# Performance work log

Hardware: AMD Instinct MI355X
Metric: run time of the kernel (lower is better)

Reference implementation:

```python
import jax, jax.numpy as jnp
import numpy as np

# --- HashGrid config (matches tcnn Encoding config in __init__) ---
N_LEVELS = 10
F = 8                       # n_features_per_level
LOG2_HASH = 20
HASH_SIZE = 1 << LOG2_HASH
BASE_RES = 16
MAX_RES = 1024
PER_LEVEL_SCALE = float(np.exp((np.log(MAX_RES) - np.log(BASE_RES)) / (N_LEVELS - 1)))
FEAT_DIM = 768
HIDDEN = FEAT_DIM // 2
N_POINTS = 131072

_PRIMES = (1, 2654435761)   # tcnn 2D spatial hash primes
_CORNERS = np.array([[0, 0], [1, 0], [0, 1], [1, 1]], dtype=np.uint32)


def _level_res(l):
    # tcnn: scale = base * growth^l - 1 ; resolution = ceil(scale) + 1
    scale = BASE_RES * PER_LEVEL_SCALE ** l - 1.0
    res = int(np.ceil(scale)) + 1
    return scale, res


def hashgrid_encode(coords, table):
    """coords: [N,2] in [0,1]; table: [L, HASH_SIZE, F] -> [N, L*F]."""
    corners = jnp.asarray(_CORNERS)                      # [4,2] uint32
    feats = []
    for l in range(N_LEVELS):
        scale, res = _level_res(l)
        pos = coords * jnp.float32(scale) + 0.5          # [N,2]
        pos_grid = jnp.floor(pos)
        frac = pos - pos_grid                            # [N,2]
        pg = pos_grid.astype(jnp.uint32)                 # [N,2]
        cpos = pg[:, None, :] + corners[None]            # [N,4,2]
        if res * res <= HASH_SIZE:
            # dense level: row-major index fits in the table
            idx = cpos[..., 0] + cpos[..., 1] * jnp.uint32(res)
        else:
            # spatial hash: (x*p0) ^ (y*p1) & (T-1)
            idx = (cpos[..., 0] * jnp.uint32(_PRIMES[0])) ^ (cpos[..., 1] * jnp.uint32(_PRIMES[1]))
            idx = idx & jnp.uint32(HASH_SIZE - 1)
        # bilinear weights: prod over dims of (frac if corner==1 else 1-frac)
        cf = corners[None].astype(frac.dtype)            # [1,4,2]
        w2 = jnp.where(cf == 1.0, frac[:, None, :], 1.0 - frac[:, None, :])  # [N,4,2]
        w = w2[..., 0] * w2[..., 1]                      # [N,4]
        lv = table[l][idx.astype(jnp.int32)]             # [N,4,F] irregular gather
        feats.append(jnp.einsum('nc,ncf->nf', w, lv))    # [N,F]
    return jnp.concatenate(feats, axis=-1)               # [N, L*F]


def setup_inputs() -> dict:
    key = jax.random.key(0)
    k0, k1, k2, k3 = jax.random.split(key, 4)
    coords = jax.random.uniform(k0, (N_POINTS, 2), dtype=jnp.float32)
    # tcnn initializes hash tables uniform in [-1e-4, 1e-4]
    table = jax.random.uniform(k1, (N_LEVELS, HASH_SIZE, F), dtype=jnp.float32,
                               minval=-1e-4, maxval=1e-4)
    in_dim = N_LEVELS * F
    w1 = jax.random.normal(k2, (in_dim, HIDDEN), dtype=jnp.float32) / np.sqrt(in_dim)
    b1 = jnp.zeros((HIDDEN,), dtype=jnp.float32)
    w2 = jax.random.normal(k3, (HIDDEN, FEAT_DIM), dtype=jnp.float32) / np.sqrt(HIDDEN)
    b2 = jnp.zeros((FEAT_DIM,), dtype=jnp.float32)
    return {"coords": coords, "table": table, "w1": w1, "b1": b1, "w2": w2, "b2": b2}


def reference(coords, table, w1, b1, w2, b2):
    enc = hashgrid_encode(coords, table)                 # [N, 80]
    h = jax.nn.relu(enc @ w1 + b1)                       # [N, 384]
    return h @ w2 + b2                                   # [N, 768]
```

## Files before the change

kernel.cpp:

```cpp
#include <hip/hip_runtime.h>
#include <cmath>

typedef short short8 __attribute__((ext_vector_type(8)));
typedef unsigned short u16x8 __attribute__((ext_vector_type(8)));
typedef float f32x4 __attribute__((ext_vector_type(4)));

struct EncParams { float scale[10]; int res[10]; };

__device__ __forceinline__ unsigned short f2bf(float f) {
  unsigned u = __builtin_bit_cast(unsigned, f);
  return (unsigned short)((u + 0x7FFFu + ((u >> 16) & 1u)) >> 16);
}

__device__ __forceinline__ void enc_level(float x, float y, float sc, int res,
    const float* __restrict__ table, int l, unsigned short* er) {
  float posx = __fadd_rn(__fmul_rn(x, sc), 0.5f);
  float posy = __fadd_rn(__fmul_rn(y, sc), 0.5f);
  float gx = floorf(posx), gy = floorf(posy);
  float fx = posx - gx, fy = posy - gy;
  unsigned px = (unsigned)gx, py = (unsigned)gy;
  unsigned idx[4];
  if (res * res <= (1 << 20)) {
    unsigned b = px + py * (unsigned)res;
    idx[0] = b; idx[1] = b + 1u;
    idx[2] = b + (unsigned)res; idx[3] = b + (unsigned)res + 1u;
  } else {
    unsigned hy0 = py * 2654435761u;
    unsigned hy1 = hy0 + 2654435761u;
    idx[0] = (px ^ hy0) & 0xFFFFFu;
    idx[1] = ((px + 1u) ^ hy0) & 0xFFFFFu;
    idx[2] = (px ^ hy1) & 0xFFFFFu;
    idx[3] = ((px + 1u) ^ hy1) & 0xFFFFFu;
  }
  float omx = 1.0f - fx, omy = 1.0f - fy;
  float w[4] = { omx * omy, fx * omy, omx * fy, fx * fy };
  const float4* tl = reinterpret_cast<const float4*>(table) + ((size_t)l << 21);
  float acc[8] = {0.f,0.f,0.f,0.f,0.f,0.f,0.f,0.f};
#pragma unroll
  for (int c = 0; c < 4; ++c) {
    float4 lo = tl[2 * (size_t)idx[c]];
    float4 hi = tl[2 * (size_t)idx[c] + 1];
    float wc = w[c];
    acc[0] = fmaf(wc, lo.x, acc[0]); acc[1] = fmaf(wc, lo.y, acc[1]);
    acc[2] = fmaf(wc, lo.z, acc[2]); acc[3] = fmaf(wc, lo.w, acc[3]);
    acc[4] = fmaf(wc, hi.x, acc[4]); acc[5] = fmaf(wc, hi.y, acc[5]);
    acc[6] = fmaf(wc, hi.z, acc[6]); acc[7] = fmaf(wc, hi.w, acc[7]);
  }
  u16x8 o;
#pragma unroll
  for (int j = 0; j < 8; ++j) o[j] = f2bf(acc[j]);
  *reinterpret_cast<u16x8*>(er + 8 * l) = o;
}

__global__ __launch_bounds__(512, 2) void nf_main(
    const float* __restrict__ coords, const float* __restrict__ table,
    const float* __restrict__ w1, const float* __restrict__ w2,
    const float* __restrict__ b1v, const float* __restrict__ b2v,
    float* __restrict__ out, EncParams P) {
  __shared__ __align__(16) unsigned short encS[128][104];
  __shared__ __align__(16) unsigned short hS[128][392];
  const int tid = threadIdx.x;
  const size_t rowBase = (size_t)blockIdx.x * 128;

  {
    const int p = tid & 127, g = tid >> 7;
    float2 c = reinterpret_cast<const float2*>(coords)[rowBase + p];
    unsigned short* er = &encS[p][0];
    if (g == 0) {
      enc_level(c.x, c.y, P.scale[0], P.res[0], table, 0, er);
      enc_level(c.x, c.y, P.scale[4], P.res[4], table, 4, er);
      enc_level(c.x, c.y, P.scale[8], P.res[8], table, 8, er);
    } else if (g == 1) {
      enc_level(c.x, c.y, P.scale[1], P.res[1], table, 1, er);
      enc_level(c.x, c.y, P.scale[5], P.res[5], table, 5, er);
      enc_level(c.x, c.y, P.scale[9], P.res[9], table, 9, er);
    } else if (g == 2) {
      enc_level(c.x, c.y, P.scale[2], P.res[2], table, 2, er);
      enc_level(c.x, c.y, P.scale[6], P.res[6], table, 6, er);
      u16x8 z = {};
      *reinterpret_cast<u16x8*>(er + 80) = z;
    } else {
      enc_level(c.x, c.y, P.scale[3], P.res[3], table, 3, er);
      enc_level(c.x, c.y, P.scale[7], P.res[7], table, 7, er);
      u16x8 z = {};
      *reinterpret_cast<u16x8*>(er + 88) = z;
    }
  }
  __syncthreads();

  const int lane = tid & 63, wv = tid >> 6;
  const int lr = lane & 15, lhi = lane >> 4;

  f32x4 acc1[8][3];
#pragma unroll
  for (int ri = 0; ri < 8; ++ri)
#pragma unroll
    for (int cf = 0; cf < 3; ++cf) acc1[ri][cf] = (f32x4){0.f, 0.f, 0.f, 0.f};
#pragma unroll
  for (int ks = 0; ks < 3; ++ks) {
    short8 a[8];
#pragma unroll
    for (int ri = 0; ri < 8; ++ri)
      a[ri] = *reinterpret_cast<const short8*>(&encS[16 * ri + lr][32 * ks + 8 * lhi]);
#pragma unroll
    for (int cf = 0; cf < 3; ++cf) {
      const int colB = 48 * wv + 16 * cf + lr;
      short8 b;
#pragma unroll
      for (int j = 0; j < 8; ++j) {
        int k = 32 * ks + 8 * lhi + j;
        b[j] = (k < 80) ? (short)f2bf(w1[(size_t)k * 384 + colB]) : (short)0;
      }
#pragma unroll
      for (int ri = 0; ri < 8; ++ri)
        acc1[ri][cf] = __builtin_amdgcn_mfma_f32_16x16x32_bf16(a[ri], b, acc1[ri][cf], 0, 0, 0);
    }
  }
#pragma unroll
  for (int ri = 0; ri < 8; ++ri)
#pragma unroll
    for (int cf = 0; cf < 3; ++cf) {
      int col = 48 * wv + 16 * cf + lr;
      float bb = b1v[col];
#pragma unroll
      for (int j = 0; j < 4; ++j) {
        int r = 16 * ri + 4 * lhi + j;
        float v = acc1[ri][cf][j] + bb;
        hS[r][col] = f2bf(fmaxf(v, 0.0f));
      }
    }
  __syncthreads();

#pragma unroll
  for (int cc = 0; cc < 2; ++cc) {
    f32x4 acc[8][3];
#pragma unroll
    for (int ri = 0; ri < 8; ++ri)
#pragma unroll
      for (int cf = 0; cf < 3; ++cf) acc[ri][cf] = (f32x4){0.f, 0.f, 0.f, 0.f};
#pragma unroll
    for (int ks = 0; ks < 12; ++ks) {
      short8 a[8];
#pragma unroll
      for (int ri = 0; ri < 8; ++ri)
        a[ri] = *reinterpret_cast<const short8*>(&hS[16 * ri + lr][32 * ks + 8 * lhi]);
#pragma unroll
      for (int cf = 0; cf < 3; ++cf) {
        const int colB = 96 * wv + 48 * cc + 16 * cf + lr;
        short8 b;
#pragma unroll
        for (int j = 0; j < 8; ++j) {
          int k = 32 * ks + 8 * lhi + j;
          b[j] = (short)f2bf(w2[(size_t)k * 768 + colB]);
        }
#pragma unroll
        for (int ri = 0; ri < 8; ++ri)
          acc[ri][cf] = __builtin_amdgcn_mfma_f32_16x16x32_bf16(a[ri], b, acc[ri][cf], 0, 0, 0);
      }
    }
#pragma unroll
    for (int ri = 0; ri < 8; ++ri)
#pragma unroll
      for (int cf = 0; cf < 3; ++cf) {
        int col = 96 * wv + 48 * cc + 16 * cf + lr;
        float bb = b2v[col];
#pragma unroll
        for (int j = 0; j < 4; ++j) {
          int r = 16 * ri + 4 * lhi + j;
          out[(rowBase + r) * 768 + col] = acc[ri][cf][j] + bb;
        }
      }
  }
}

extern "C" void kernel_launch(void* const* d_in, const int* in_sizes, int n_in,
                              void* d_out, int out_size, void* d_ws, size_t ws_size,
                              hipStream_t stream) {
  const float* coords = (const float*)d_in[0];
  const float* table  = (const float*)d_in[1];
  const float* w1     = (const float*)d_in[2];
  const float* b1     = (const float*)d_in[3];
  const float* w2     = (const float*)d_in[4];
  const float* b2     = (const float*)d_in[5];
  float* out = (float*)d_out;

  EncParams P;
  double pls = exp((log(1024.0) - log(16.0)) / 9.0);
  static const int RES[10] = {16, 26, 41, 65, 102, 162, 257, 407, 646, 1025};
  for (int l = 0; l < 10; ++l) {
    double sc = 16.0 * pow(pls, (double)l) - 1.0;
    P.scale[l] = (float)sc;
    P.res[l] = RES[l];
  }

  nf_main<<<1024, 512, 0, stream>>>(coords, table, w1, w2, b1, b2, out, P);
}
```

Measured before the change: 291.0 us.

## Batch hash-grid gathers and software-prefetch MLP weights ahead of MFMA

The encoder now computes indices for all of a thread's levels first and issues every table gather before any accumulation, so more loads are in flight at once. The W1 fragments are loaded before the barrier, overlapping with the encoding phase. In the second GEMM, the W2 fragments for the next k-step are prefetched into registers while the current step's MFMAs run. This targets global-load latency stalls but raises register pressure, which could cause spills under the 512-thread, 2-block launch bound.

```diff
diff --git a/kernel.cpp b/kernel.cpp
--- a/kernel.cpp
+++ b/kernel.cpp
@@ -12,44 +12,62 @@
   return (unsigned short)((u + 0x7FFFu + ((u >> 16) & 1u)) >> 16);
 }
 
-__device__ __forceinline__ void enc_level(float x, float y, float sc, int res,
-    const float* __restrict__ table, int l, unsigned short* er) {
-  float posx = __fadd_rn(__fmul_rn(x, sc), 0.5f);
-  float posy = __fadd_rn(__fmul_rn(y, sc), 0.5f);
-  float gx = floorf(posx), gy = floorf(posy);
-  float fx = posx - gx, fy = posy - gy;
-  unsigned px = (unsigned)gx, py = (unsigned)gy;
-  unsigned idx[4];
-  if (res * res <= (1 << 20)) {
-    unsigned b = px + py * (unsigned)res;
-    idx[0] = b; idx[1] = b + 1u;
-    idx[2] = b + (unsigned)res; idx[3] = b + (unsigned)res + 1u;
-  } else {
-    unsigned hy0 = py * 2654435761u;
-    unsigned hy1 = hy0 + 2654435761u;
-    idx[0] = (px ^ hy0) & 0xFFFFFu;
-    idx[1] = ((px + 1u) ^ hy0) & 0xFFFFFu;
-    idx[2] = (px ^ hy1) & 0xFFFFFu;
-    idx[3] = ((px + 1u) ^ hy1) & 0xFFFFFu;
-  }
-  float omx = 1.0f - fx, omy = 1.0f - fy;
-  float w[4] = { omx * omy, fx * omy, omx * fy, fx * fy };
-  const float4* tl = reinterpret_cast<const float4*>(table) + ((size_t)l << 21);
-  float acc[8] = {0.f,0.f,0.f,0.f,0.f,0.f,0.f,0.f};
-#pragma unroll
-  for (int c = 0; c < 4; ++c) {
-    float4 lo = tl[2 * (size_t)idx[c]];
-    float4 hi = tl[2 * (size_t)idx[c] + 1];
-    float wc = w[c];
-    acc[0] = fmaf(wc, lo.x, acc[0]); acc[1] = fmaf(wc, lo.y, acc[1]);
-    acc[2] = fmaf(wc, lo.z, acc[2]); acc[3] = fmaf(wc, lo.w, acc[3]);
-    acc[4] = fmaf(wc, hi.x, acc[4]); acc[5] = fmaf(wc, hi.y, acc[5]);
-    acc[6] = fmaf(wc, hi.z, acc[6]); acc[7] = fmaf(wc, hi.w, acc[7]);
-  }
-  u16x8 o;
-#pragma unroll
-  for (int j = 0; j < 8; ++j) o[j] = f2bf(acc[j]);
-  *reinterpret_cast<u16x8*>(er + 8 * l) = o;
+template<int NL>
+__device__ __forceinline__ void enc_levels(const float* __restrict__ table,
+    float x, float y, const float* sc, const int* rs, const int* lid,
+    unsigned short* er) {
+  unsigned idx[NL][4];
+  float w[NL][4];
+#pragma unroll
+  for (int t = 0; t < NL; ++t) {
+    float posx = __fadd_rn(__fmul_rn(x, sc[t]), 0.5f);
+    float posy = __fadd_rn(__fmul_rn(y, sc[t]), 0.5f);
+    float gx = floorf(posx), gy = floorf(posy);
+    float fx = posx - gx, fy = posy - gy;
+    unsigned px = (unsigned)gx, py = (unsigned)gy;
+    int res = rs[t];
+    if (res * res <= (1 << 20)) {
+      unsigned b = px + py * (unsigned)res;
+      idx[t][0] = b; idx[t][1] = b + 1u;
+      idx[t][2] = b + (unsigned)res; idx[t][3] = b + (unsigned)res + 1u;
+    } else {
+      unsigned hy0 = py * 2654435761u;
+      unsigned hy1 = hy0 + 2654435761u;
+      idx[t][0] = (px ^ hy0) & 0xFFFFFu;
+      idx[t][1] = ((px + 1u) ^ hy0) & 0xFFFFFu;
+      idx[t][2] = (px ^ hy1) & 0xFFFFFu;
+      idx[t][3] = ((px + 1u) ^ hy1) & 0xFFFFFu;
+    }
+    float omx = 1.0f - fx, omy = 1.0f - fy;
+    w[t][0] = omx * omy; w[t][1] = fx * omy;
+    w[t][2] = omx * fy;  w[t][3] = fx * fy;
+  }
+  float4 v[NL][4][2];
+#pragma unroll
+  for (int t = 0; t < NL; ++t) {
+    const float4* tl = reinterpret_cast<const float4*>(table) + ((size_t)lid[t] << 21);
+#pragma unroll
+    for (int c = 0; c < 4; ++c) {
+      v[t][c][0] = tl[2 * (size_t)idx[t][c]];
+      v[t][c][1] = tl[2 * (size_t)idx[t][c] + 1];
+    }
+  }
+#pragma unroll
+  for (int t = 0; t < NL; ++t) {
+    float acc[8] = {0.f,0.f,0.f,0.f,0.f,0.f,0.f,0.f};
+#pragma unroll
+    for (int c = 0; c < 4; ++c) {
+      float wc = w[t][c];
+      acc[0] = fmaf(wc, v[t][c][0].x, acc[0]); acc[1] = fmaf(wc, v[t][c][0].y, acc[1]);
+      acc[2] = fmaf(wc, v[t][c][0].z, acc[2]); acc[3] = fmaf(wc, v[t][c][0].w, acc[3]);
+      acc[4] = fmaf(wc, v[t][c][1].x, acc[4]); acc[5] = fmaf(wc, v[t][c][1].y, acc[5]);
+      acc[6] = fmaf(wc, v[t][c][1].z, acc[6]); acc[7] = fmaf(wc, v[t][c][1].w, acc[7]);
+    }
+    u16x8 o;
+#pragma unroll
+    for (int j = 0; j < 8; ++j) o[j] = f2bf(acc[j]);
+    *reinterpret_cast<u16x8*>(er + 8 * lid[t]) = o;
+  }
 }
 
 __global__ __launch_bounds__(512, 2) void nf_main(
@@ -61,35 +79,53 @@
   __shared__ __align__(16) unsigned short hS[128][392];
   const int tid = threadIdx.x;
   const size_t rowBase = (size_t)blockIdx.x * 128;
+  const int lane = tid & 63, wv = tid >> 6;
+  const int lr = lane & 15, lhi = lane >> 4;
 
   {
     const int p = tid & 127, g = tid >> 7;
     float2 c = reinterpret_cast<const float2*>(coords)[rowBase + p];
     unsigned short* er = &encS[p][0];
     if (g == 0) {
-      enc_level(c.x, c.y, P.scale[0], P.res[0], table, 0, er);
-      enc_level(c.x, c.y, P.scale[4], P.res[4], table, 4, er);
-      enc_level(c.x, c.y, P.scale[8], P.res[8], table, 8, er);
+      const int L[3] = {0, 4, 8};
+      const float sc[3] = {P.scale[0], P.scale[4], P.scale[8]};
+      const int rs[3] = {P.res[0], P.res[4], P.res[8]};
+      enc_levels<3>(table, c.x, c.y, sc, rs, L, er);
     } else if (g == 1) {
-      enc_level(c.x, c.y, P.scale[1], P.res[1], table, 1, er);
-      enc_level(c.x, c.y, P.scale[5], P.res[5], table, 5, er);
-      enc_level(c.x, c.y, P.scale[9], P.res[9], table, 9, er);
+      const int L[3] = {1, 5, 9};
+      const float sc[3] = {P.scale[1], P.scale[5], P.scale[9]};
+      const int rs[3] = {P.res[1], P.res[5], P.res[9]};
+      enc_levels<3>(table, c.x, c.y, sc, rs, L, er);
     } else if (g == 2) {
-      enc_level(c.x, c.y, P.scale[2], P.res[2], table, 2, er);
-      enc_level(c.x, c.y, P.scale[6], P.res[6], table, 6, er);
+      const int L[2] = {2, 6};
+      const float sc[2] = {P.scale[2], P.scale[6]};
+      const int rs[2] = {P.res[2], P.res[6]};
+      enc_levels<2>(table, c.x, c.y, sc, rs, L, er);
       u16x8 z = {};
       *reinterpret_cast<u16x8*>(er + 80) = z;
     } else {
-      enc_level(c.x, c.y, P.scale[3], P.res[3], table, 3, er);
-      enc_level(c.x, c.y, P.scale[7], P.res[7], table, 7, er);
+      const int L[2] = {3, 7};
+      const float sc[2] = {P.scale[3], P.scale[7]};
+      const int rs[2] = {P.res[3], P.res[7]};
+      enc_levels<2>(table, c.x, c.y, sc, rs, L, er);
       u16x8 z = {};
       *reinterpret_cast<u16x8*>(er + 88) = z;
     }
   }
+
+  short8 bW1[3][3];
+#pragma unroll
+  for (int ks = 0; ks < 3; ++ks)
+#pragma unroll
+    for (int cf = 0; cf < 3; ++cf) {
+      const int colB = 48 * wv + 16 * cf + lr;
+#pragma unroll
+      for (int j = 0; j < 8; ++j) {
+        int k = 32 * ks + 8 * lhi + j;
+        bW1[ks][cf][j] = (k < 80) ? (short)f2bf(w1[(size_t)k * 384 + colB]) : (short)0;
+      }
+    }
   __syncthreads();
-
-  const int lane = tid & 63, wv = tid >> 6;
-  const int lr = lane & 15, lhi = lane >> 4;
 
   f32x4 acc1[8][3];
 #pragma unroll
@@ -103,18 +139,10 @@
     for (int ri = 0; ri < 8; ++ri)
       a[ri] = *reinterpret_cast<const short8*>(&encS[16 * ri + lr][32 * ks + 8 * lhi]);
 #pragma unroll
-    for (int cf = 0; cf < 3; ++cf) {
-      const int colB = 48 * wv + 16 * cf + lr;
-      short8 b;
-#pragma unroll
-      for (int j = 0; j < 8; ++j) {
-        int k = 32 * ks + 8 * lhi + j;
-        b[j] = (k < 80) ? (short)f2bf(w1[(size_t)k * 384 + colB]) : (short)0;
-      }
+    for (int cf = 0; cf < 3; ++cf)
 #pragma unroll
       for (int ri = 0; ri < 8; ++ri)
-        acc1[ri][cf] = __builtin_amdgcn_mfma_f32_16x16x32_bf16(a[ri], b, acc1[ri][cf], 0, 0, 0);
-    }
+        acc1[ri][cf] = __builtin_amdgcn_mfma_f32_16x16x32_bf16(a[ri], bW1[ks][cf], acc1[ri][cf], 0, 0, 0);
   }
 #pragma unroll
   for (int ri = 0; ri < 8; ++ri)
@@ -138,25 +166,41 @@
     for (int ri = 0; ri < 8; ++ri)
 #pragma unroll
       for (int cf = 0; cf < 3; ++cf) acc[ri][cf] = (f32x4){0.f, 0.f, 0.f, 0.f};
+
+    float wnxt[3][8];
+#pragma unroll
+    for (int cf = 0; cf < 3; ++cf) {
+      const int colB = 96 * wv + 48 * cc + 16 * cf + lr;
+#pragma unroll
+      for (int j = 0; j < 8; ++j)
+        wnxt[cf][j] = w2[(size_t)(8 * lhi + j) * 768 + colB];
+    }
 #pragma unroll
     for (int ks = 0; ks < 12; ++ks) {
       short8 a[8];
 #pragma unroll
       for (int ri = 0; ri < 8; ++ri)
         a[ri] = *reinterpret_cast<const short8*>(&hS[16 * ri + lr][32 * ks + 8 * lhi]);
-#pragma unroll
-      for (int cf = 0; cf < 3; ++cf) {
-        const int colB = 96 * wv + 48 * cc + 16 * cf + lr;
-        short8 b;
-#pragma unroll
-        for (int j = 0; j < 8; ++j) {
-          int k = 32 * ks + 8 * lhi + j;
-          b[j] = (short)f2bf(w2[(size_t)k * 768 + colB]);
+      short8 b[3];
+#pragma unroll
+      for (int cf = 0; cf < 3; ++cf)
+#pragma unroll
+        for (int j = 0; j < 8; ++j)
+          b[cf][j] = (short)f2bf(wnxt[cf][j]);
+      if (ks < 11) {
+#pragma unroll
+        for (int cf = 0; cf < 3; ++cf) {
+          const int colB = 96 * wv + 48 * cc + 16 * cf + lr;
+#pragma unroll
+          for (int j = 0; j < 8; ++j)
+            wnxt[cf][j] = w2[(size_t)(32 * (ks + 1) + 8 * lhi + j) * 768 + colB];
         }
+      }
+#pragma unroll
+      for (int cf = 0; cf < 3; ++cf)
 #pragma unroll
         for (int ri = 0; ri < 8; ++ri)
-          acc[ri][cf] = __builtin_amdgcn_mfma_f32_16x16x32_bf16(a[ri], b, acc[ri][cf], 0, 0, 0);
-      }
+          acc[ri][cf] = __builtin_amdgcn_mfma_f32_16x16x32_bf16(a[ri], b[cf], acc[ri][cf], 0, 0, 0);
     }
 #pragma unroll
     for (int ri = 0; ri < 8; ++ri)
```

Measured after the change: 300.2 us. 1.03x slower.
